# Performance work log

Hardware: AMD Instinct MI355X
Metric: run time of the kernel (lower is better)

The kernel has to match this reference:

```python
import jax, jax.numpy as jnp
import numpy as np

C = 256
POOL = 4

def setup_inputs() -> dict:
    key = jax.random.key(0)
    ks = jax.random.split(key, 8)
    B, H, W = 4, 256, 256
    d = C // 8
    x = jax.random.normal(ks[0], (B, C, H, W), dtype=jnp.float32)
    # 1x1 conv weights stored as [out, in] matrices (kernel_size=1)
    s = 1.0 / np.sqrt(C)
    Wq = jax.random.uniform(ks[1], (d, C), jnp.float32, -s, s)
    bq = jax.random.uniform(ks[2], (d,), jnp.float32, -s, s)
    Wk = jax.random.uniform(ks[3], (d, C), jnp.float32, -s, s)
    bk = jax.random.uniform(ks[4], (d,), jnp.float32, -s, s)
    Wv = jax.random.uniform(ks[5], (C, C), jnp.float32, -s, s)
    bv = jax.random.uniform(ks[6], (C,), jnp.float32, -s, s)
    gamma = jax.random.normal(ks[7], (1,), jnp.float32) * 0.1
    return {"x": x, "Wq": Wq, "bq": bq, "Wk": Wk, "bk": bk,
            "Wv": Wv, "bv": bv, "gamma": gamma}


def reference(x, Wq, bq, Wk, bk, Wv, bv, gamma):
    B, Cc, H, W = x.shape
    Hp, Wp = H // POOL, W // POOL
    # AvgPool2d(kernel=4, stride=4)
    xp = x.reshape(B, Cc, Hp, POOL, Wp, POOL).mean(axis=(3, 5))  # [B,C,Hp,Wp]
    xf = xp.reshape(B, Cc, Hp * Wp)                              # [B,C,N]
    # 1x1 convs == channel matmuls
    q = jnp.einsum('dc,bcn->bdn', Wq, xf) + bq[None, :, None]    # [B,d,N]
    k = jnp.einsum('dc,bcn->bdn', Wk, xf) + bk[None, :, None]    # [B,d,N]
    v = jnp.einsum('ec,bcn->ben', Wv, xf) + bv[None, :, None]    # [B,C,N]
    # energy[b,n,m] = q[:, :, n] . k[:, :, m]
    energy = jnp.einsum('bdn,bdm->bnm', q, k)                    # [B,N,N]
    attn = jax.nn.softmax(energy, axis=-1)
    # out = v @ attn^T  -> out[b,c,n] = sum_m v[b,c,m] * attn[b,n,m]
    out = jnp.einsum('bcm,bnm->bcn', v, attn)                    # [B,C,N]
    out = out.reshape(B, Cc, Hp, Wp)
    # bilinear upsample, half-pixel centers (align_corners=False)
    up = jax.image.resize(out, (B, Cc, H, W), method='bilinear')
    return gamma[0] * up + x
```

## Files before the change

### kernel.cpp

```cpp
#include <hip/hip_runtime.h>

#define B_ 4
#define C_ 256
#define N_ 4096
#define D_ 32

typedef __bf16 bf16;
typedef __bf16 bf16x4 __attribute__((ext_vector_type(4)));
typedef __bf16 bf16x8 __attribute__((ext_vector_type(8)));
typedef float f32x4 __attribute__((ext_vector_type(4)));

__global__ __launch_bounds__(256) void k_prep(
    const float* __restrict__ Wq, const float* __restrict__ bq,
    const float* __restrict__ Wk, const float* __restrict__ bk,
    const float* __restrict__ Wv, const float* __restrict__ bv,
    bf16* __restrict__ wt, float* __restrict__ bias) {
  int r = blockIdx.x, t = threadIdx.x;
  const float* src; float bval;
  if (r < 32)      { src = Wq + (r << 8);        bval = bq[r]; }
  else if (r < 64) { src = Wk + ((r - 32) << 8); bval = bk[r - 32]; }
  else             { src = Wv + ((r - 64) << 8); bval = bv[r - 64]; }
  wt[(r << 8) + t] = (bf16)src[t];
  if (t == 0) bias[r] = bval;
}

__global__ __launch_bounds__(1024) void k_fused(const float* __restrict__ x,
    const bf16* __restrict__ wt, const float* __restrict__ bias,
    bf16* __restrict__ qt, bf16* __restrict__ kt, bf16* __restrict__ v) {
  __shared__ bf16 xsb[64][264];
  int tid = threadIdx.x, wave = tid >> 6, l = tid & 63;
  int lg = l >> 4, ll = l & 15;
  int b = blockIdx.x >> 6, hp = blockIdx.x & 63, n0 = hp * 64;

  const float4* x4 = reinterpret_cast<const float4*>(x) +
      ((size_t)((b * 256 + wave * 16) * 256 + hp * 4)) * 64 + l;
  for (int c0 = 0; c0 < 16; c0 += 4) {
    float s[4] = {0.f, 0.f, 0.f, 0.f};
    #pragma unroll
    for (int j = 0; j < 4; ++j) {
      const float4* p = x4 + (size_t)(c0 + j) * 16384;
      #pragma unroll
      for (int dh = 0; dh < 4; ++dh) {
        float4 a = p[dh * 64];
        s[j] += a.x + a.y + a.z + a.w;
      }
    }
    bf16x4 pk;
    #pragma unroll
    for (int j = 0; j < 4; ++j) pk[j] = (bf16)(s[j] * 0.0625f);
    *reinterpret_cast<bf16x4*>(&xsb[l][wave * 16 + c0]) = pk;
  }
  __syncthreads();

  f32x4 acc[2][4];
  #pragma unroll
  for (int j = 0; j < 2; ++j)
    #pragma unroll
    for (int cb = 0; cb < 4; ++cb) acc[j][cb] = (f32x4){0.f, 0.f, 0.f, 0.f};

  for (int kk = 0; kk < 8; ++kk) {
    bf16x8 bfr[4];
    #pragma unroll
    for (int cb = 0; cb < 4; ++cb)
      bfr[cb] = *reinterpret_cast<const bf16x8*>(&xsb[cb * 16 + ll][kk * 32 + lg * 8]);
    #pragma unroll
    for (int j = 0; j < 2; ++j) {
      int rb = wave + j * 16;
      if (rb < 20) {
        bf16x8 afr = *reinterpret_cast<const bf16x8*>(
            wt + ((size_t)(rb * 16 + ll)) * 256 + kk * 32 + lg * 8);
        #pragma unroll
        for (int cb = 0; cb < 4; ++cb)
          acc[j][cb] = __builtin_amdgcn_mfma_f32_16x16x32_bf16(afr, bfr[cb], acc[j][cb], 0, 0, 0);
      }
    }
  }

  #pragma unroll
  for (int j = 0; j < 2; ++j) {
    int rb = wave + j * 16;
    if (rb < 20) {
      int row0 = rb * 16 + lg * 4;
      float4 b4 = *reinterpret_cast<const float4*>(bias + row0);
      #pragma unroll
      for (int cb = 0; cb < 4; ++cb) {
        int n = n0 + cb * 16 + ll;
        float v0 = acc[j][cb][0] + b4.x, v1 = acc[j][cb][1] + b4.y;
        float v2 = acc[j][cb][2] + b4.z, v3 = acc[j][cb][3] + b4.w;
        if (row0 < 32) {
          bf16x4 pk = {(bf16)v0, (bf16)v1, (bf16)v2, (bf16)v3};
          *reinterpret_cast<bf16x4*>(qt + ((size_t)(b * N_ + n)) * D_ + row0) = pk;
        } else if (row0 < 64) {
          bf16x4 pk = {(bf16)v0, (bf16)v1, (bf16)v2, (bf16)v3};
          *reinterpret_cast<bf16x4*>(kt + ((size_t)(b * N_ + n)) * D_ + row0 - 32) = pk;
        } else {
          int c = row0 - 64;
          v[((size_t)(b * 256 + c + 0)) * N_ + n] = (bf16)v0;
          v[((size_t)(b * 256 + c + 1)) * N_ + n] = (bf16)v1;
          v[((size_t)(b * 256 + c + 2)) * N_ + n] = (bf16)v2;
          v[((size_t)(b * 256 + c + 3)) * N_ + n] = (bf16)v3;
        }
      }
    }
  }
}

__global__ __launch_bounds__(1024) void k_attn(const bf16* __restrict__ qt,
    const bf16* __restrict__ kt, const bf16* __restrict__ v,
    float* __restrict__ outs) {
  __shared__ bf16 p_s[2][64][264];
  __shared__ float l_red[16][64];
  __shared__ float l_s[64];
  int tid = threadIdx.x, wave = tid >> 6, l = tid & 63;
  int lg = l >> 4, ll = l & 15;
  int blk = blockIdx.x;
  int b  = (blk & 7) >> 1;
  int nt = ((blk >> 3) << 1) | (blk & 1);
  int n0 = nt * 64;

  const f32x4 fz = {0.f, 0.f, 0.f, 0.f};

  bf16x8 aq[4];
  #pragma unroll
  for (int tnf = 0; tnf < 4; ++tnf)
    aq[tnf] = *reinterpret_cast<const bf16x8*>(
        qt + ((size_t)(b * N_ + n0 + tnf * 16 + ll)) * D_ + lg * 8);

  f32x4 acc[4];
  float lsum[4][4];
  #pragma unroll
  for (int a = 0; a < 4; ++a) {
    acc[a] = fz;
    #pragma unroll
    for (int r = 0; r < 4; ++r) lsum[a][r] = 0.f;
  }

  const int mw = wave * 16;
  const int colw = mw + ll;

  {
    bf16x8 bk8 = *reinterpret_cast<const bf16x8*>(
        kt + ((size_t)(b * N_ + colw)) * D_ + lg * 8);
    #pragma unroll
    for (int tnf = 0; tnf < 4; ++tnf) {
      f32x4 e = __builtin_amdgcn_mfma_f32_16x16x32_bf16(aq[tnf], bk8, fz, 0, 0, 0);
      #pragma unroll
      for (int r = 0; r < 4; ++r) {
        float p = __expf(e[r]);
        lsum[tnf][r] += p;
        p_s[0][tnf * 16 + lg * 4 + r][colw] = (bf16)p;
      }
    }
  }
  __syncthreads();

  for (int t = 0; t < 15; ++t) {
    int m0 = t * 256;
    int cur = t & 1, nxt = cur ^ 1;
    bf16x8 bk8 = *reinterpret_cast<const bf16x8*>(
        kt + ((size_t)(b * N_ + m0 + 256 + colw)) * D_ + lg * 8);
    #pragma unroll
    for (int kk = 0; kk < 8; ++kk) {
      bf16x8 bv8 = *reinterpret_cast<const bf16x8*>(
          v + ((size_t)((b << 8) + colw)) * N_ + m0 + kk * 32 + lg * 8);
      #pragma unroll
      for (int tnf = 0; tnf < 4; ++tnf) {
        bf16x8 pa = *reinterpret_cast<const bf16x8*>(
            &p_s[cur][tnf * 16 + ll][kk * 32 + lg * 8]);
        acc[tnf] = __builtin_amdgcn_mfma_f32_16x16x32_bf16(pa, bv8, acc[tnf], 0, 0, 0);
      }
    }
    #pragma unroll
    for (int tnf = 0; tnf < 4; ++tnf) {
      f32x4 e = __builtin_amdgcn_mfma_f32_16x16x32_bf16(aq[tnf], bk8, fz, 0, 0, 0);
      #pragma unroll
      for (int r = 0; r < 4; ++r) {
        float p = __expf(e[r]);
        lsum[tnf][r] += p;
        p_s[nxt][tnf * 16 + lg * 4 + r][colw] = (bf16)p;
      }
    }
    __syncthreads();
  }
  {
    int m0 = 15 * 256;
    #pragma unroll
    for (int kk = 0; kk < 8; ++kk) {
      bf16x8 bv8 = *reinterpret_cast<const bf16x8*>(
          v + ((size_t)((b << 8) + colw)) * N_ + m0 + kk * 32 + lg * 8);
      #pragma unroll
      for (int tnf = 0; tnf < 4; ++tnf) {
        bf16x8 pa = *reinterpret_cast<const bf16x8*>(
            &p_s[1][tnf * 16 + ll][kk * 32 + lg * 8]);
        acc[tnf] = __builtin_amdgcn_mfma_f32_16x16x32_bf16(pa, bv8, acc[tnf], 0, 0, 0);
      }
    }
  }

  #pragma unroll
  for (int tnf = 0; tnf < 4; ++tnf) {
    #pragma unroll
    for (int r = 0; r < 4; ++r) {
      float s = lsum[tnf][r];
      s += __shfl_xor(s, 1);
      s += __shfl_xor(s, 2);
      s += __shfl_xor(s, 4);
      s += __shfl_xor(s, 8);
      if (ll == 0) l_red[wave][tnf * 16 + lg * 4 + r] = s;
    }
  }
  __syncthreads();
  if (tid < 64) {
    float s = 0.f;
    #pragma unroll
    for (int w = 0; w < 16; ++w) s += l_red[w][tid];
    l_s[tid] = s;
  }
  __syncthreads();

  #pragma unroll
  for (int tnf = 0; tnf < 4; ++tnf) {
    int tn0 = tnf * 16 + lg * 4;
    float4 o;
    o.x = acc[tnf][0] / l_s[tn0 + 0];
    o.y = acc[tnf][1] / l_s[tn0 + 1];
    o.z = acc[tnf][2] / l_s[tn0 + 2];
    o.w = acc[tnf][3] / l_s[tn0 + 3];
    *reinterpret_cast<float4*>(outs + ((size_t)((b << 8) + colw)) * N_ + n0 + tn0) = o;
  }
}

__global__ __launch_bounds__(256) void k_up(const float* __restrict__ outs,
    const float* __restrict__ x, const float* __restrict__ gamma,
    float* __restrict__ out) {
  __shared__ float s_o[4096];
  int tid = threadIdx.x, wave = tid >> 6, tw = tid & 63;
  int bc = blockIdx.x;
  const float* src = outs + (size_t)bc * 4096;
  #pragma unroll
  for (int ch = 0; ch < 4; ++ch)
    *reinterpret_cast<float4*>(&s_o[ch * 1024 + tid * 4]) =
        *reinterpret_cast<const float4*>(src + ch * 1024 + tid * 4);
  __syncthreads();

  float g = gamma[0];
  const float4* xr = reinterpret_cast<const float4*>(x) + (size_t)bc * 16384;
  float4* outr = reinterpret_cast<float4*>(out) + (size_t)bc * 16384;

  int twm = tw == 0 ? 0 : tw - 1;
  int twp = tw == 63 ? 63 : tw + 1;

  for (int hb = 0; hb < 64; ++hb) {
    int h = hb * 4 + wave;
    int th = 2 * h - 3;
    int h0 = th < 0 ? -1 : (th >> 3);
    float fh = (float)(th - 8 * h0) * 0.125f;
    int i0h = h0 < 0 ? 0 : h0;
    int i1h = h0 + 1 > 63 ? 63 : h0 + 1;
    const float* r0 = &s_o[i0h * 64];
    const float* r1 = &s_o[i1h * 64];
    float a_m = r0[twm], a_c = r0[tw], a_p = r0[twp];
    float b_m = r1[twm], b_c = r1[tw], b_p = r1[twp];
    float t0 = a_m + 0.625f * (a_c - a_m), u0 = b_m + 0.625f * (b_c - b_m);
    float t1 = a_m + 0.875f * (a_c - a_m), u1 = b_m + 0.875f * (b_c - b_m);
    float t2 = a_c + 0.125f * (a_p - a_c), u2 = b_c + 0.125f * (b_p - b_c);
    float t3 = a_c + 0.375f * (a_p - a_c), u3 = b_c + 0.375f * (b_p - b_c);
    float4 xv = xr[h * 64 + tw];
    float4 o;
    o.x = g * (t0 + fh * (u0 - t0)) + xv.x;
    o.y = g * (t1 + fh * (u1 - t1)) + xv.y;
    o.z = g * (t2 + fh * (u2 - t2)) + xv.z;
    o.w = g * (t3 + fh * (u3 - t3)) + xv.w;
    outr[h * 64 + tw] = o;
  }
}

extern "C" void kernel_launch(void* const* d_in, const int* in_sizes, int n_in,
                              void* d_out, int out_size, void* d_ws, size_t ws_size,
                              hipStream_t stream) {
  const float* x     = (const float*)d_in[0];
  const float* Wq    = (const float*)d_in[1];
  const float* bq    = (const float*)d_in[2];
  const float* Wk    = (const float*)d_in[3];
  const float* bk    = (const float*)d_in[4];
  const float* Wv    = (const float*)d_in[5];
  const float* bv    = (const float*)d_in[6];
  const float* gamma = (const float*)d_in[7];
  float* out = (float*)d_out;

  char* ws = (char*)d_ws;
  float* outs = (float*)(ws);
  bf16*  v    = (bf16*) (ws + (16u << 20));
  bf16*  qt   = (bf16*) (ws + (24u << 20));
  bf16*  kt   = (bf16*) (ws + (25u << 20));
  bf16*  wt   = (bf16*) (ws + (26u << 20));
  float* bias = (float*)(ws + (27u << 20));

  hipLaunchKernelGGL(k_prep,  dim3(320),  dim3(256),  0, stream,
                     Wq, bq, Wk, bk, Wv, bv, wt, bias);
  hipLaunchKernelGGL(k_fused, dim3(256),  dim3(1024), 0, stream,
                     x, wt, bias, qt, kt, v);
  hipLaunchKernelGGL(k_attn,  dim3(256),  dim3(1024), 0, stream, qt, kt, v, outs);
  hipLaunchKernelGGL(k_up,    dim3(1024), dim3(256),  0, stream, outs, x, gamma, out);
}
```

Before: 253.1 us.

## Split PV matmul across key-range wave groups with register tiling and LDS reduction

Each wave now owns a 64-channel by 64-key slice of the PV product and keeps a 4x4 block of MFMA accumulators, instead of 16 channels over all 256 keys. This lets each loaded P fragment and V fragment be reused across four MFMAs, cutting LDS and global loads per MFMA. The four key-group partial sums are then reduced through a new 48KB shared buffer, with extra barriers in the epilogue. The cost is higher register pressure (64 accumulator floats per lane) and more LDS, which may reduce occupancy.

```diff
diff --git a/kernel.cpp b/kernel.cpp
--- a/kernel.cpp
+++ b/kernel.cpp
@@ -109,6 +109,7 @@
     const bf16* __restrict__ kt, const bf16* __restrict__ v,
     float* __restrict__ outs) {
   __shared__ bf16 p_s[2][64][264];
+  __shared__ float red_s[12 * 1024];
   __shared__ float l_red[16][64];
   __shared__ float l_s[64];
   int tid = threadIdx.x, wave = tid >> 6, l = tid & 63;
@@ -126,17 +127,21 @@
     aq[tnf] = *reinterpret_cast<const bf16x8*>(
         qt + ((size_t)(b * N_ + n0 + tnf * 16 + ll)) * D_ + lg * 8);
 
-  f32x4 acc[4];
+  f32x4 acc[4][4];
   float lsum[4][4];
   #pragma unroll
   for (int a = 0; a < 4; ++a) {
-    acc[a] = fz;
+    #pragma unroll
+    for (int cf = 0; cf < 4; ++cf) acc[a][cf] = fz;
     #pragma unroll
     for (int r = 0; r < 4; ++r) lsum[a][r] = 0.f;
   }
 
   const int mw = wave * 16;
   const int colw = mw + ll;
+  const int cb = wave >> 2, g = wave & 3;
+  const int cw = cb * 64, mg = g * 64;
+  const bf16* vbase = v + ((size_t)(b << 8)) * N_;
 
   {
     bf16x8 bk8 = *reinterpret_cast<const bf16x8*>(
@@ -160,15 +165,23 @@
     bf16x8 bk8 = *reinterpret_cast<const bf16x8*>(
         kt + ((size_t)(b * N_ + m0 + 256 + colw)) * D_ + lg * 8);
     #pragma unroll
-    for (int kk = 0; kk < 8; ++kk) {
-      bf16x8 bv8 = *reinterpret_cast<const bf16x8*>(
-          v + ((size_t)((b << 8) + colw)) * N_ + m0 + kk * 32 + lg * 8);
-      #pragma unroll
-      for (int tnf = 0; tnf < 4; ++tnf) {
-        bf16x8 pa = *reinterpret_cast<const bf16x8*>(
-            &p_s[cur][tnf * 16 + ll][kk * 32 + lg * 8]);
-        acc[tnf] = __builtin_amdgcn_mfma_f32_16x16x32_bf16(pa, bv8, acc[tnf], 0, 0, 0);
-      }
+    for (int kk = 0; kk < 2; ++kk) {
+      int mk = m0 + mg + kk * 32 + lg * 8;
+      bf16x8 bv[4];
+      #pragma unroll
+      for (int cf = 0; cf < 4; ++cf)
+        bv[cf] = *reinterpret_cast<const bf16x8*>(
+            vbase + ((size_t)(cw + cf * 16 + ll)) * N_ + mk);
+      bf16x8 pa[4];
+      #pragma unroll
+      for (int tnf = 0; tnf < 4; ++tnf)
+        pa[tnf] = *reinterpret_cast<const bf16x8*>(
+            &p_s[cur][tnf * 16 + ll][mg + kk * 32 + lg * 8]);
+      #pragma unroll
+      for (int tnf = 0; tnf < 4; ++tnf)
+        #pragma unroll
+        for (int cf = 0; cf < 4; ++cf)
+          acc[tnf][cf] = __builtin_amdgcn_mfma_f32_16x16x32_bf16(pa[tnf], bv[cf], acc[tnf][cf], 0, 0, 0);
     }
     #pragma unroll
     for (int tnf = 0; tnf < 4; ++tnf) {
@@ -185,15 +198,23 @@
   {
     int m0 = 15 * 256;
     #pragma unroll
-    for (int kk = 0; kk < 8; ++kk) {
-      bf16x8 bv8 = *reinterpret_cast<const bf16x8*>(
-          v + ((size_t)((b << 8) + colw)) * N_ + m0 + kk * 32 + lg * 8);
-      #pragma unroll
-      for (int tnf = 0; tnf < 4; ++tnf) {
-        bf16x8 pa = *reinterpret_cast<const bf16x8*>(
-            &p_s[1][tnf * 16 + ll][kk * 32 + lg * 8]);
-        acc[tnf] = __builtin_amdgcn_mfma_f32_16x16x32_bf16(pa, bv8, acc[tnf], 0, 0, 0);
-      }
+    for (int kk = 0; kk < 2; ++kk) {
+      int mk = m0 + mg + kk * 32 + lg * 8;
+      bf16x8 bv[4];
+      #pragma unroll
+      for (int cf = 0; cf < 4; ++cf)
+        bv[cf] = *reinterpret_cast<const bf16x8*>(
+            vbase + ((size_t)(cw + cf * 16 + ll)) * N_ + mk);
+      bf16x8 pa[4];
+      #pragma unroll
+      for (int tnf = 0; tnf < 4; ++tnf)
+        pa[tnf] = *reinterpret_cast<const bf16x8*>(
+            &p_s[1][tnf * 16 + ll][mg + kk * 32 + lg * 8]);
+      #pragma unroll
+      for (int tnf = 0; tnf < 4; ++tnf)
+        #pragma unroll
+        for (int cf = 0; cf < 4; ++cf)
+          acc[tnf][cf] = __builtin_amdgcn_mfma_f32_16x16x32_bf16(pa[tnf], bv[cf], acc[tnf][cf], 0, 0, 0);
     }
   }
 
@@ -216,17 +237,43 @@
     for (int w = 0; w < 16; ++w) s += l_red[w][tid];
     l_s[tid] = s;
   }
-  __syncthreads();
 
   #pragma unroll
   for (int tnf = 0; tnf < 4; ++tnf) {
-    int tn0 = tnf * 16 + lg * 4;
-    float4 o;
-    o.x = acc[tnf][0] / l_s[tn0 + 0];
-    o.y = acc[tnf][1] / l_s[tn0 + 1];
-    o.z = acc[tnf][2] / l_s[tn0 + 2];
-    o.w = acc[tnf][3] / l_s[tn0 + 3];
-    *reinterpret_cast<float4*>(outs + ((size_t)((b << 8) + colw)) * N_ + n0 + tn0) = o;
+    if (g > 0) {
+      float* dst = &red_s[((g - 1) * 4 + cb) * 1024 + l * 16];
+      #pragma unroll
+      for (int cf = 0; cf < 4; ++cf)
+        *reinterpret_cast<f32x4*>(dst + cf * 4) = acc[tnf][cf];
+    }
+    __syncthreads();
+    if (g == 0) {
+      #pragma unroll
+      for (int p = 0; p < 3; ++p) {
+        const float* srcp = &red_s[(p * 4 + cb) * 1024 + l * 16];
+        #pragma unroll
+        for (int cf = 0; cf < 4; ++cf)
+          acc[tnf][cf] += *reinterpret_cast<const f32x4*>(srcp + cf * 4);
+      }
+    }
+    __syncthreads();
+  }
+
+  if (g == 0) {
+    #pragma unroll
+    for (int tnf = 0; tnf < 4; ++tnf) {
+      int tn0 = tnf * 16 + lg * 4;
+      #pragma unroll
+      for (int cf = 0; cf < 4; ++cf) {
+        int c = cw + cf * 16 + ll;
+        float4 o;
+        o.x = acc[tnf][cf][0] / l_s[tn0 + 0];
+        o.y = acc[tnf][cf][1] / l_s[tn0 + 1];
+        o.z = acc[tnf][cf][2] / l_s[tn0 + 2];
+        o.w = acc[tnf][cf][3] / l_s[tn0 + 3];
+        *reinterpret_cast<float4*>(outs + ((size_t)((b << 8) + c)) * N_ + n0 + tn0) = o;
+      }
+    }
   }
 }
 
```

Result: slower. 279.5 us (+10.4%).

## Transpose QK MFMA and XOR-swizzle P tile for vectorized LDS stores

Applied to the files above, without the earlier changes.

Swaps the MFMA operand order for the QK^T product so each lane holds four consecutive key columns of one query row. This lets the exp'd probabilities be packed and written to shared memory as a single bf16x4 store instead of four scalar bf16 stores. The P tile drops its padding and uses an XOR swizzle on 8-element blocks to avoid bank conflicts on both the writes and the bf16x8 reads. The row-sum reduction also shrinks from 16 per-lane partials with four shuffles each to 4 partials with two shuffles, at the cost of extra index arithmetic and the risk of getting the swizzle mapping wrong.

```diff
diff --git a/kernel.cpp b/kernel.cpp
--- a/kernel.cpp
+++ b/kernel.cpp
@@ -108,7 +108,7 @@
 __global__ __launch_bounds__(1024) void k_attn(const bf16* __restrict__ qt,
     const bf16* __restrict__ kt, const bf16* __restrict__ v,
     float* __restrict__ outs) {
-  __shared__ bf16 p_s[2][64][264];
+  __shared__ bf16 p_s[2][64][256];
   __shared__ float l_red[16][64];
   __shared__ float l_s[64];
   int tid = threadIdx.x, wave = tid >> 6, l = tid & 63;
@@ -127,29 +127,33 @@
         qt + ((size_t)(b * N_ + n0 + tnf * 16 + ll)) * D_ + lg * 8);
 
   f32x4 acc[4];
-  float lsum[4][4];
-  #pragma unroll
-  for (int a = 0; a < 4; ++a) {
-    acc[a] = fz;
-    #pragma unroll
-    for (int r = 0; r < 4; ++r) lsum[a][r] = 0.f;
-  }
+  float lsum[4];
+  #pragma unroll
+  for (int a = 0; a < 4; ++a) { acc[a] = fz; lsum[a] = 0.f; }
 
   const int mw = wave * 16;
   const int colw = mw + ll;
+  const bf16* vbase = v + ((size_t)(b << 8)) * N_;
+
+  const int st_blk = 2 * wave + (lg >> 1);
+  const int st_el  = (lg & 1) * 4;
 
   {
     bf16x8 bk8 = *reinterpret_cast<const bf16x8*>(
         kt + ((size_t)(b * N_ + colw)) * D_ + lg * 8);
     #pragma unroll
     for (int tnf = 0; tnf < 4; ++tnf) {
-      f32x4 e = __builtin_amdgcn_mfma_f32_16x16x32_bf16(aq[tnf], bk8, fz, 0, 0, 0);
+      f32x4 e = __builtin_amdgcn_mfma_f32_16x16x32_bf16(bk8, aq[tnf], fz, 0, 0, 0);
+      int row = tnf * 16 + ll;
+      bf16x4 pk;
       #pragma unroll
       for (int r = 0; r < 4; ++r) {
         float p = __expf(e[r]);
-        lsum[tnf][r] += p;
-        p_s[0][tnf * 16 + lg * 4 + r][colw] = (bf16)p;
-      }
+        lsum[tnf] += p;
+        pk[r] = (bf16)p;
+      }
+      int col = ((st_blk ^ (row & 7)) << 3) + st_el;
+      *reinterpret_cast<bf16x4*>(&p_s[0][row][col]) = pk;
     }
   }
   __syncthreads();
@@ -162,23 +166,28 @@
     #pragma unroll
     for (int kk = 0; kk < 8; ++kk) {
       bf16x8 bv8 = *reinterpret_cast<const bf16x8*>(
-          v + ((size_t)((b << 8) + colw)) * N_ + m0 + kk * 32 + lg * 8);
+          vbase + ((size_t)colw) * N_ + m0 + kk * 32 + lg * 8);
       #pragma unroll
       for (int tnf = 0; tnf < 4; ++tnf) {
-        bf16x8 pa = *reinterpret_cast<const bf16x8*>(
-            &p_s[cur][tnf * 16 + ll][kk * 32 + lg * 8]);
+        int row = tnf * 16 + ll;
+        int col = (((kk * 4 + lg) ^ (ll & 7)) << 3);
+        bf16x8 pa = *reinterpret_cast<const bf16x8*>(&p_s[cur][row][col]);
         acc[tnf] = __builtin_amdgcn_mfma_f32_16x16x32_bf16(pa, bv8, acc[tnf], 0, 0, 0);
       }
     }
     #pragma unroll
     for (int tnf = 0; tnf < 4; ++tnf) {
-      f32x4 e = __builtin_amdgcn_mfma_f32_16x16x32_bf16(aq[tnf], bk8, fz, 0, 0, 0);
+      f32x4 e = __builtin_amdgcn_mfma_f32_16x16x32_bf16(bk8, aq[tnf], fz, 0, 0, 0);
+      int row = tnf * 16 + ll;
+      bf16x4 pk;
       #pragma unroll
       for (int r = 0; r < 4; ++r) {
         float p = __expf(e[r]);
-        lsum[tnf][r] += p;
-        p_s[nxt][tnf * 16 + lg * 4 + r][colw] = (bf16)p;
-      }
+        lsum[tnf] += p;
+        pk[r] = (bf16)p;
+      }
+      int col = ((st_blk ^ (row & 7)) << 3) + st_el;
+      *reinterpret_cast<bf16x4*>(&p_s[nxt][row][col]) = pk;
     }
     __syncthreads();
   }
@@ -187,11 +196,12 @@
     #pragma unroll
     for (int kk = 0; kk < 8; ++kk) {
       bf16x8 bv8 = *reinterpret_cast<const bf16x8*>(
-          v + ((size_t)((b << 8) + colw)) * N_ + m0 + kk * 32 + lg * 8);
+          vbase + ((size_t)colw) * N_ + m0 + kk * 32 + lg * 8);
       #pragma unroll
       for (int tnf = 0; tnf < 4; ++tnf) {
-        bf16x8 pa = *reinterpret_cast<const bf16x8*>(
-            &p_s[1][tnf * 16 + ll][kk * 32 + lg * 8]);
+        int row = tnf * 16 + ll;
+        int col = (((kk * 4 + lg) ^ (ll & 7)) << 3);
+        bf16x8 pa = *reinterpret_cast<const bf16x8*>(&p_s[1][row][col]);
         acc[tnf] = __builtin_amdgcn_mfma_f32_16x16x32_bf16(pa, bv8, acc[tnf], 0, 0, 0);
       }
     }
@@ -199,15 +209,10 @@
 
   #pragma unroll
   for (int tnf = 0; tnf < 4; ++tnf) {
-    #pragma unroll
-    for (int r = 0; r < 4; ++r) {
-      float s = lsum[tnf][r];
-      s += __shfl_xor(s, 1);
-      s += __shfl_xor(s, 2);
-      s += __shfl_xor(s, 4);
-      s += __shfl_xor(s, 8);
-      if (ll == 0) l_red[wave][tnf * 16 + lg * 4 + r] = s;
-    }
+    float s = lsum[tnf];
+    s += __shfl_xor(s, 16);
+    s += __shfl_xor(s, 32);
+    if (l < 16) l_red[wave][tnf * 16 + l] = s;
   }
   __syncthreads();
   if (tid < 64) {
```

Result: faster. 248.2 us (-2.0%).
